# Kernel optimization log

Measured on AMD Instinct MI355X. Metric: run time of the kernel, lower is better.

The kernel has to match this reference:

```python
import jax, jax.numpy as jnp
import numpy as np

BETA = 0.5
TEMPERATURE = 1.0
IGNORE_INDEX = -100
BT, H, V = 2048, 2048, 32000


def setup_inputs() -> dict:
    key = jax.random.key(0)
    k1, k2, k3, k4, k5 = jax.random.split(key, 5)
    return {
        "student_input": jax.random.normal(k1, (BT, H), dtype=jnp.float32),
        "student_weight": jax.random.normal(k2, (V, H), dtype=jnp.float32) * 0.02,
        "teacher_input": jax.random.normal(k3, (BT, H), dtype=jnp.float32),
        "teacher_weight": jax.random.normal(k4, (V, H), dtype=jnp.float32) * 0.02,
        "labels": jax.random.randint(k5, (BT,), 0, V, dtype=jnp.int64),
    }


def reference(student_input, student_weight, teacher_input, teacher_weight, labels):
    # logits = x @ W^T, scaled by temperature, then log-softmax (computed in fp32)
    s_logits = jnp.einsum("bh,vh->bv", student_input, student_weight).astype(jnp.float32)
    t_logits = jnp.einsum("bh,vh->bv", teacher_input, teacher_weight).astype(jnp.float32)
    s_lp = jax.nn.log_softmax(s_logits / TEMPERATURE, axis=-1)  # log Q, (BT, V)
    t_lp = jax.nn.log_softmax(t_logits / TEMPERATURE, axis=-1)  # log P, (BT, V)
    Q = jnp.exp(s_lp)
    P = jnp.exp(t_lp)
    # generalized JSD: M = beta*P + (1-beta)*Q
    log_m = jnp.log(BETA * P + (1.0 - BETA) * Q)
    per_row = jnp.sum(BETA * P * (t_lp - log_m) + (1.0 - BETA) * Q * (s_lp - log_m), axis=-1)  # (BT,)
    valid = (labels != IGNORE_INDEX)
    n_non_ignore = jnp.maximum(jnp.sum(valid), 1).astype(jnp.float32)
    loss = jnp.sum(jnp.where(valid, per_row, 0.0)) / n_non_ignore
    return loss
```

## Files before the change

kernel.cpp:

```cpp
#include <hip/hip_runtime.h>
#include <stdint.h>

#define BT 2048
#define H  2048
#define V  32000

typedef __attribute__((ext_vector_type(8))) short short8;
typedef __attribute__((ext_vector_type(4))) float f32x4;

__device__ inline unsigned short f2bf(float x) {
  unsigned int u = __float_as_uint(x);
  u += 0x7FFFu + ((u >> 16) & 1u);
  return (unsigned short)(u >> 16);
}

__global__ __launch_bounds__(256) void zero_ws(float* rowsum, float* accum) {
  int i = blockIdx.x * blockDim.x + threadIdx.x;
  if (i < 2 * BT) rowsum[i] = 0.0f;
  if (i == 0) {
    accum[0] = 0.0f;
    ((unsigned int*)accum)[1] = 0u;
  }
}

__global__ __launch_bounds__(256) void cvt_kernel(const float* __restrict__ src,
                                                  unsigned short* __restrict__ dst,
                                                  int n8) {
  int i = blockIdx.x * blockDim.x + threadIdx.x;
  if (i >= n8) return;
  const float4* s = (const float4*)src;
  float4 a = s[2 * i];
  float4 b = s[2 * i + 1];
  union { unsigned short us[8]; uint4 v; } o;
  o.us[0] = f2bf(a.x); o.us[1] = f2bf(a.y); o.us[2] = f2bf(a.z); o.us[3] = f2bf(a.w);
  o.us[4] = f2bf(b.x); o.us[5] = f2bf(b.y); o.us[6] = f2bf(b.z); o.us[7] = f2bf(b.w);
  ((uint4*)dst)[i] = o.v;
}

#define BM 128
#define BN 128
#define BK 32

__global__ __launch_bounds__(256) void gemm_bt(const unsigned short* __restrict__ A0,
                                               const unsigned short* __restrict__ B0,
                                               const unsigned short* __restrict__ A1,
                                               const unsigned short* __restrict__ B1,
                                               unsigned short* __restrict__ C0,
                                               unsigned short* __restrict__ C1,
                                               float* __restrict__ rowsum) {
  const int z = blockIdx.z;
  const unsigned short* A = z ? A1 : A0;
  const unsigned short* B = z ? B1 : B0;
  unsigned short* C = z ? C1 : C0;
  float* rs = rowsum + z * BT;

  const int m0 = blockIdx.x * BM;
  const int n0 = blockIdx.y * BN;

  __shared__ alignas(16) unsigned short lA[BM * BK];
  __shared__ alignas(16) unsigned short lB[BN * BK];

  const int tid  = threadIdx.x;
  const int lane = tid & 63;
  const int w    = tid >> 6;
  const int wm   = w & 1;
  const int wn   = w >> 1;

  f32x4 acc[4][4];
  #pragma unroll
  for (int i = 0; i < 4; i++)
    #pragma unroll
    for (int j = 0; j < 4; j++)
      acc[i][j] = (f32x4){0.f, 0.f, 0.f, 0.f};

  const int q  = lane >> 4;
  const int l4 = lane & 15;

  for (int k0 = 0; k0 < H; k0 += BK) {
    #pragma unroll
    for (int i = 0; i < 2; i++) {
      int basec = (i * 4 + w) * 64;
      int c     = basec + lane;
      int row   = c >> 2;
      int cq    = (c & 3) ^ (row & 3);
      const unsigned short* ga = A + (size_t)(m0 + row) * H + k0 + cq * 8;
      const unsigned short* gb = B + (size_t)(n0 + row) * H + k0 + cq * 8;
      __builtin_amdgcn_global_load_lds(
          (const __attribute__((address_space(1))) unsigned int*)ga,
          (__attribute__((address_space(3))) unsigned int*)&lA[basec * 8], 16, 0, 0);
      __builtin_amdgcn_global_load_lds(
          (const __attribute__((address_space(1))) unsigned int*)gb,
          (__attribute__((address_space(3))) unsigned int*)&lB[basec * 8], 16, 0, 0);
    }
    __syncthreads();

    short8 af[4], bf[4];
    #pragma unroll
    for (int mi = 0; mi < 4; mi++) {
      int M = wm * 64 + mi * 16 + l4;
      af[mi] = *(const short8*)&lA[(M * 4 + (q ^ (M & 3))) * 8];
    }
    #pragma unroll
    for (int ni = 0; ni < 4; ni++) {
      int N = wn * 64 + ni * 16 + l4;
      bf[ni] = *(const short8*)&lB[(N * 4 + (q ^ (N & 3))) * 8];
    }

    #pragma unroll
    for (int mi = 0; mi < 4; mi++)
      #pragma unroll
      for (int ni = 0; ni < 4; ni++)
        acc[mi][ni] = __builtin_amdgcn_mfma_f32_16x16x32_bf16(af[mi], bf[ni], acc[mi][ni], 0, 0, 0);

    __syncthreads();
  }

  #pragma unroll
  for (int mi = 0; mi < 4; mi++)
    #pragma unroll
    for (int ni = 0; ni < 4; ni++)
      #pragma unroll
      for (int r = 0; r < 4; r++) {
        int gr = m0 + wm * 64 + mi * 16 + q * 4 + r;
        int gc = n0 + wn * 64 + ni * 16 + l4;
        C[(size_t)gr * V + gc] = f2bf(acc[mi][ni][r]);
      }

  #pragma unroll
  for (int mi = 0; mi < 4; mi++) {
    #pragma unroll
    for (int r = 0; r < 4; r++) {
      float s = 0.f;
      #pragma unroll
      for (int ni = 0; ni < 4; ni++) s += __expf(acc[mi][ni][r]);
      #pragma unroll
      for (int o = 1; o < 16; o <<= 1) s += __shfl_xor(s, o, 64);
      if (l4 == 0) {
        int gr = m0 + wm * 64 + mi * 16 + q * 4 + r;
        atomicAdd(&rs[gr], s);
      }
    }
  }
}

__device__ inline void unpack8(uint4 v, float* f) {
  f[0] = __uint_as_float(v.x << 16);
  f[1] = __uint_as_float(v.x & 0xFFFF0000u);
  f[2] = __uint_as_float(v.y << 16);
  f[3] = __uint_as_float(v.y & 0xFFFF0000u);
  f[4] = __uint_as_float(v.z << 16);
  f[5] = __uint_as_float(v.z & 0xFFFF0000u);
  f[6] = __uint_as_float(v.w << 16);
  f[7] = __uint_as_float(v.w & 0xFFFF0000u);
}

__global__ __launch_bounds__(256) void jsd_kernel(const unsigned short* __restrict__ Slog,
                                                  const unsigned short* __restrict__ Tlog,
                                                  const float* __restrict__ rowsum,
                                                  const long long* __restrict__ labels,
                                                  float* __restrict__ accum) {
  const int r   = blockIdx.x;
  const int tid = threadIdx.x;
  __shared__ float red[4];

  const uint4* s4 = (const uint4*)(Slog + (size_t)r * V);
  const uint4* t4 = (const uint4*)(Tlog + (size_t)r * V);
  const int NC = V / 8;

  const float slse = __logf(rowsum[r]);
  const float tlse = __logf(rowsum[BT + r]);

  float loss = 0.f;
  for (int c = tid; c < NC; c += 256) {
    uint4 sv = s4[c], tv = t4[c];
    float fs[8], ft[8];
    unpack8(sv, fs); unpack8(tv, ft);
    #pragma unroll
    for (int j = 0; j < 8; j++) {
      float sl = fs[j] - slse;
      float tl = ft[j] - tlse;
      float qv = __expf(sl);
      float pv = __expf(tl);
      float m  = 0.5f * (pv + qv);
      float lm = __logf(m);
      loss += 0.5f * (pv * (tl - lm) + qv * (sl - lm));
    }
  }
  #pragma unroll
  for (int o = 32; o > 0; o >>= 1) loss += __shfl_xor(loss, o, 64);
  if ((tid & 63) == 0) red[tid >> 6] = loss;
  __syncthreads();
  if (tid == 0) {
    loss = (red[0] + red[1]) + (red[2] + red[3]);
    long long lab = labels[r];
    if (lab != -100LL) {
      atomicAdd(&accum[0], loss);
      atomicAdd((unsigned int*)&accum[1], 1u);
    }
  }
}

__global__ void finalize(const float* __restrict__ accum, float* __restrict__ out) {
  float cnt = (float)((const unsigned int*)accum)[1];
  out[0] = accum[0] / fmaxf(cnt, 1.0f);
}

extern "C" void kernel_launch(void* const* d_in, const int* in_sizes, int n_in,
                              void* d_out, int out_size, void* d_ws, size_t ws_size,
                              hipStream_t stream) {
  const float* s_in = (const float*)d_in[0];
  const float* s_w  = (const float*)d_in[1];
  const float* t_in = (const float*)d_in[2];
  const float* t_w  = (const float*)d_in[3];
  const long long* labels = (const long long*)d_in[4];
  float* out = (float*)d_out;

  char* ws = (char*)d_ws;
  size_t off = 0;
  auto take = [&](size_t bytes) -> char* {
    char* p = ws + off;
    off += (bytes + 255) & ~(size_t)255;
    return p;
  };
  unsigned short* sw_bf = (unsigned short*)take((size_t)V * H * 2);
  unsigned short* tw_bf = (unsigned short*)take((size_t)V * H * 2);
  unsigned short* si_bf = (unsigned short*)take((size_t)BT * H * 2);
  unsigned short* ti_bf = (unsigned short*)take((size_t)BT * H * 2);
  unsigned short* slog  = (unsigned short*)take((size_t)BT * V * 2);
  unsigned short* tlog  = (unsigned short*)take((size_t)BT * V * 2);
  float* rowsum = (float*)take((size_t)2 * BT * 4);
  float* accum  = (float*)take(256);
  if (off > ws_size) return;

  zero_ws<<<dim3((2 * BT + 255) / 256), dim3(256), 0, stream>>>(rowsum, accum);

  const int nW8 = (V * H) / 8;
  const int nI8 = (BT * H) / 8;
  cvt_kernel<<<dim3((nW8 + 255) / 256), dim3(256), 0, stream>>>(s_w, sw_bf, nW8);
  cvt_kernel<<<dim3((nW8 + 255) / 256), dim3(256), 0, stream>>>(t_w, tw_bf, nW8);
  cvt_kernel<<<dim3((nI8 + 255) / 256), dim3(256), 0, stream>>>(s_in, si_bf, nI8);
  cvt_kernel<<<dim3((nI8 + 255) / 256), dim3(256), 0, stream>>>(t_in, ti_bf, nI8);

  gemm_bt<<<dim3(BT / BM, V / BN, 2), dim3(256), 0, stream>>>(si_bf, sw_bf, ti_bf, tw_bf,
                                                              slog, tlog, rowsum);

  jsd_kernel<<<dim3(BT), dim3(256), 0, stream>>>(slog, tlog, rowsum, labels, accum);

  finalize<<<dim3(1), dim3(1), 0, stream>>>(accum, out);
}
```

Baseline: 1.508 ms.

## Merge conversion launches, fold finalize into JSD, drop LDS swizzle, add nontemporal IO

Merges the zero-init and four conversion kernels into one launch, and replaces the separate finalize kernel with a last-block ticket inside the JSD kernel. It also removes the XOR swizzle from the GEMM's LDS layout, fuses the exp row-sum into the bf16 store loop, and uses nontemporal stores and loads for the logits. The aim is to cut launch overhead and cache pollution. Dropping the swizzle risks LDS bank conflicts on the fragment reads.

New measurement: 1.439 ms. 4.5% less time.

```diff
diff --git a/kernel.cpp b/kernel.cpp
--- a/kernel.cpp
+++ b/kernel.cpp
@@ -7,6 +7,7 @@
 
 typedef __attribute__((ext_vector_type(8))) short short8;
 typedef __attribute__((ext_vector_type(4))) float f32x4;
+typedef __attribute__((ext_vector_type(4))) unsigned int u32x4;
 
 __device__ inline unsigned short f2bf(float x) {
   unsigned int u = __float_as_uint(x);
@@ -14,27 +15,37 @@
   return (unsigned short)(u >> 16);
 }
 
-__global__ __launch_bounds__(256) void zero_ws(float* rowsum, float* accum) {
-  int i = blockIdx.x * blockDim.x + threadIdx.x;
-  if (i < 2 * BT) rowsum[i] = 0.0f;
-  if (i == 0) {
-    accum[0] = 0.0f;
-    ((unsigned int*)accum)[1] = 0u;
-  }
-}
-
-__global__ __launch_bounds__(256) void cvt_kernel(const float* __restrict__ src,
-                                                  unsigned short* __restrict__ dst,
-                                                  int n8) {
-  int i = blockIdx.x * blockDim.x + threadIdx.x;
-  if (i >= n8) return;
-  const float4* s = (const float4*)src;
-  float4 a = s[2 * i];
-  float4 b = s[2 * i + 1];
+#define W8 (V * H / 8)
+#define I8 (BT * H / 8)
+__global__ __launch_bounds__(256) void cvt_all(const float* __restrict__ s_w,
+                                               const float* __restrict__ t_w,
+                                               const float* __restrict__ s_in,
+                                               const float* __restrict__ t_in,
+                                               unsigned short* __restrict__ sw_bf,
+                                               unsigned short* __restrict__ tw_bf,
+                                               unsigned short* __restrict__ si_bf,
+                                               unsigned short* __restrict__ ti_bf,
+                                               float* __restrict__ rowsum,
+                                               float* __restrict__ accum) {
+  const int tid = threadIdx.x;
+  if (blockIdx.x == 0) {
+    for (int j = tid; j < 2 * BT; j += 256) rowsum[j] = 0.0f;
+    if (tid < 4) ((unsigned int*)accum)[tid] = 0u;
+  }
+  long long i = (long long)blockIdx.x * 256 + tid;
+  const float4* src;
+  uint4* dst;
+  if (i < W8)                    { src = (const float4*)s_w;  dst = (uint4*)sw_bf; }
+  else if (i < 2LL * W8)         { src = (const float4*)t_w;  dst = (uint4*)tw_bf; i -= W8; }
+  else if (i < 2LL * W8 + I8)    { src = (const float4*)s_in; dst = (uint4*)si_bf; i -= 2LL * W8; }
+  else if (i < 2LL * W8 + 2 * I8){ src = (const float4*)t_in; dst = (uint4*)ti_bf; i -= 2LL * W8 + I8; }
+  else return;
+  float4 a = src[2 * i];
+  float4 b = src[2 * i + 1];
   union { unsigned short us[8]; uint4 v; } o;
   o.us[0] = f2bf(a.x); o.us[1] = f2bf(a.y); o.us[2] = f2bf(a.z); o.us[3] = f2bf(a.w);
   o.us[4] = f2bf(b.x); o.us[5] = f2bf(b.y); o.us[6] = f2bf(b.z); o.us[7] = f2bf(b.w);
-  ((uint4*)dst)[i] = o.v;
+  dst[i] = o.v;
 }
 
 #define BM 128
@@ -82,7 +93,7 @@
       int basec = (i * 4 + w) * 64;
       int c     = basec + lane;
       int row   = c >> 2;
-      int cq    = (c & 3) ^ (row & 3);
+      int cq    = c & 3;
       const unsigned short* ga = A + (size_t)(m0 + row) * H + k0 + cq * 8;
       const unsigned short* gb = B + (size_t)(n0 + row) * H + k0 + cq * 8;
       __builtin_amdgcn_global_load_lds(
@@ -98,12 +109,12 @@
     #pragma unroll
     for (int mi = 0; mi < 4; mi++) {
       int M = wm * 64 + mi * 16 + l4;
-      af[mi] = *(const short8*)&lA[(M * 4 + (q ^ (M & 3))) * 8];
+      af[mi] = *(const short8*)&lA[(M * 4 + q) * 8];
     }
     #pragma unroll
     for (int ni = 0; ni < 4; ni++) {
       int N = wn * 64 + ni * 16 + l4;
-      bf[ni] = *(const short8*)&lB[(N * 4 + (q ^ (N & 3))) * 8];
+      bf[ni] = *(const short8*)&lB[(N * 4 + q) * 8];
     }
 
     #pragma unroll
@@ -116,55 +127,55 @@
   }
 
   #pragma unroll
-  for (int mi = 0; mi < 4; mi++)
-    #pragma unroll
-    for (int ni = 0; ni < 4; ni++)
+  for (int mi = 0; mi < 4; mi++) {
+    float s[4] = {0.f, 0.f, 0.f, 0.f};
+    #pragma unroll
+    for (int ni = 0; ni < 4; ni++) {
       #pragma unroll
       for (int r = 0; r < 4; r++) {
+        float v = acc[mi][ni][r];
         int gr = m0 + wm * 64 + mi * 16 + q * 4 + r;
         int gc = n0 + wn * 64 + ni * 16 + l4;
-        C[(size_t)gr * V + gc] = f2bf(acc[mi][ni][r]);
+        __builtin_nontemporal_store(f2bf(v), &C[(size_t)gr * V + gc]);
+        s[r] += __expf(v);
       }
-
-  #pragma unroll
-  for (int mi = 0; mi < 4; mi++) {
+    }
     #pragma unroll
     for (int r = 0; r < 4; r++) {
-      float s = 0.f;
+      float sv = s[r];
       #pragma unroll
-      for (int ni = 0; ni < 4; ni++) s += __expf(acc[mi][ni][r]);
-      #pragma unroll
-      for (int o = 1; o < 16; o <<= 1) s += __shfl_xor(s, o, 64);
+      for (int o = 1; o < 16; o <<= 1) sv += __shfl_xor(sv, o, 64);
       if (l4 == 0) {
         int gr = m0 + wm * 64 + mi * 16 + q * 4 + r;
-        atomicAdd(&rs[gr], s);
+        atomicAdd(&rs[gr], sv);
       }
     }
   }
 }
 
-__device__ inline void unpack8(uint4 v, float* f) {
-  f[0] = __uint_as_float(v.x << 16);
-  f[1] = __uint_as_float(v.x & 0xFFFF0000u);
-  f[2] = __uint_as_float(v.y << 16);
-  f[3] = __uint_as_float(v.y & 0xFFFF0000u);
-  f[4] = __uint_as_float(v.z << 16);
-  f[5] = __uint_as_float(v.z & 0xFFFF0000u);
-  f[6] = __uint_as_float(v.w << 16);
-  f[7] = __uint_as_float(v.w & 0xFFFF0000u);
+__device__ inline void unpack8(u32x4 v, float* f) {
+  f[0] = __uint_as_float(v[0] << 16);
+  f[1] = __uint_as_float(v[0] & 0xFFFF0000u);
+  f[2] = __uint_as_float(v[1] << 16);
+  f[3] = __uint_as_float(v[1] & 0xFFFF0000u);
+  f[4] = __uint_as_float(v[2] << 16);
+  f[5] = __uint_as_float(v[2] & 0xFFFF0000u);
+  f[6] = __uint_as_float(v[3] << 16);
+  f[7] = __uint_as_float(v[3] & 0xFFFF0000u);
 }
 
 __global__ __launch_bounds__(256) void jsd_kernel(const unsigned short* __restrict__ Slog,
                                                   const unsigned short* __restrict__ Tlog,
                                                   const float* __restrict__ rowsum,
                                                   const long long* __restrict__ labels,
-                                                  float* __restrict__ accum) {
+                                                  float* __restrict__ accum,
+                                                  float* __restrict__ out) {
   const int r   = blockIdx.x;
   const int tid = threadIdx.x;
   __shared__ float red[4];
 
-  const uint4* s4 = (const uint4*)(Slog + (size_t)r * V);
-  const uint4* t4 = (const uint4*)(Tlog + (size_t)r * V);
+  const u32x4* s4 = (const u32x4*)(Slog + (size_t)r * V);
+  const u32x4* t4 = (const u32x4*)(Tlog + (size_t)r * V);
   const int NC = V / 8;
 
   const float slse = __logf(rowsum[r]);
@@ -172,7 +183,8 @@
 
   float loss = 0.f;
   for (int c = tid; c < NC; c += 256) {
-    uint4 sv = s4[c], tv = t4[c];
+    u32x4 sv = __builtin_nontemporal_load(&s4[c]);
+    u32x4 tv = __builtin_nontemporal_load(&t4[c]);
     float fs[8], ft[8];
     unpack8(sv, fs); unpack8(tv, ft);
     #pragma unroll
@@ -197,12 +209,14 @@
       atomicAdd(&accum[0], loss);
       atomicAdd((unsigned int*)&accum[1], 1u);
     }
-  }
-}
-
-__global__ void finalize(const float* __restrict__ accum, float* __restrict__ out) {
-  float cnt = (float)((const unsigned int*)accum)[1];
-  out[0] = accum[0] / fmaxf(cnt, 1.0f);
+    __threadfence();
+    unsigned int ticket = atomicAdd((unsigned int*)&accum[2], 1u);
+    if (ticket == BT - 1) {
+      float tot = atomicAdd(&accum[0], 0.0f);
+      unsigned int cnt = atomicAdd((unsigned int*)&accum[1], 0u);
+      out[0] = tot / fmaxf((float)cnt, 1.0f);
+    }
+  }
 }
 
 extern "C" void kernel_launch(void* const* d_in, const int* in_sizes, int n_in,
@@ -232,19 +246,12 @@
   float* accum  = (float*)take(256);
   if (off > ws_size) return;
 
-  zero_ws<<<dim3((2 * BT + 255) / 256), dim3(256), 0, stream>>>(rowsum, accum);
-
-  const int nW8 = (V * H) / 8;
-  const int nI8 = (BT * H) / 8;
-  cvt_kernel<<<dim3((nW8 + 255) / 256), dim3(256), 0, stream>>>(s_w, sw_bf, nW8);
-  cvt_kernel<<<dim3((nW8 + 255) / 256), dim3(256), 0, stream>>>(t_w, tw_bf, nW8);
-  cvt_kernel<<<dim3((nI8 + 255) / 256), dim3(256), 0, stream>>>(s_in, si_bf, nI8);
-  cvt_kernel<<<dim3((nI8 + 255) / 256), dim3(256), 0, stream>>>(t_in, ti_bf, nI8);
+  const long long total8 = 2LL * W8 + 2LL * I8;
+  cvt_all<<<dim3((unsigned)((total8 + 255) / 256)), dim3(256), 0, stream>>>(
+      s_w, t_w, s_in, t_in, sw_bf, tw_bf, si_bf, ti_bf, rowsum, accum);
 
   gemm_bt<<<dim3(BT / BM, V / BN, 2), dim3(256), 0, stream>>>(si_bf, sw_bf, ti_bf, tw_bf,
                                                               slog, tlog, rowsum);
 
-  jsd_kernel<<<dim3(BT), dim3(256), 0, stream>>>(slog, tlog, rowsum, labels, accum);
-
-  finalize<<<dim3(1), dim3(1), 0, stream>>>(accum, out);
-}
+  jsd_kernel<<<dim3(BT), dim3(256), 0, stream>>>(slog, tlog, rowsum, labels, accum, out);
+}
```
